# Performance work log

Hardware: AMD Instinct MI355X
Metric: run time of the kernel (lower is better)

The kernel has to match this reference:

```python
import jax, jax.numpy as jnp
import numpy as np

B, IH, IW = 16, 32, 32
N = IH * IW
HEADS, DIM_HEAD = 8, 64
INNER = HEADS * DIM_HEAD  # 512
INP, OUP = 512, 512
SCALE = DIM_HEAD ** -0.5


def _relative_index():
    # replicate torch.meshgrid (ij) -> coords [2, N]
    yy, xx = np.meshgrid(np.arange(IH), np.arange(IW), indexing='ij')
    coords = np.stack([yy.reshape(-1), xx.reshape(-1)])  # [2, N]
    rel = coords[:, :, None] - coords[:, None, :]        # [2, N, N]
    rel[0] += IH - 1
    rel[1] += IW - 1
    rel[0] *= 2 * IW - 1
    return jnp.asarray(rel.sum(0).reshape(-1), dtype=jnp.int32)  # [N*N]


def setup_inputs() -> dict:
    key = jax.random.key(0)
    k1, k2, k3, k4, k5 = jax.random.split(key, 5)
    x = jax.random.normal(k1, (B, N, INP), dtype=jnp.float32)
    W_qkv = jax.random.normal(k2, (INP, 3 * INNER), dtype=jnp.float32) * (INP ** -0.5)
    # table is initialized to zeros in the module; use small randn so bias path is exercised
    rel_table = jax.random.normal(k3, ((2 * IH - 1) * (2 * IW - 1), HEADS), dtype=jnp.float32) * 0.02
    W_out = jax.random.normal(k4, (INNER, OUP), dtype=jnp.float32) * (INNER ** -0.5)
    b_out = jax.random.normal(k5, (OUP,), dtype=jnp.float32) * 0.02
    return {
        'x': x,
        'W_qkv': W_qkv,
        'rel_table': rel_table,
        'W_out': W_out,
        'b_out': b_out,
        'rel_index': _relative_index(),
    }


def reference(x, W_qkv, rel_table, W_out, b_out, rel_index):
    b, n, _ = x.shape
    qkv = x @ W_qkv                                            # [b, n, 3*inner]
    q, k, v = jnp.split(qkv, 3, axis=-1)
    def to_heads(t):
        return t.reshape(b, n, HEADS, DIM_HEAD).transpose(0, 2, 1, 3)  # [b, h, n, d]
    q, k, v = to_heads(q), to_heads(k), to_heads(v)
    dots = jnp.einsum('bhnd,bhmd->bhnm', q, k) * SCALE         # [b, h, n, n]
    bias = rel_table[rel_index].reshape(n, n, HEADS).transpose(2, 0, 1)[None]  # [1, h, n, n]
    attn = jax.nn.softmax(dots + bias, axis=-1)
    out = jnp.einsum('bhnm,bhmd->bhnd', attn, v)               # [b, h, n, d]
    out = out.transpose(0, 2, 1, 3).reshape(b, n, INNER)       # [b, n, inner]
    return out @ W_out + b_out
```

## Files before the change

### kernel.cpp

```cpp
#include <hip/hip_runtime.h>
#include <math.h>

#define BATCH 16
#define NTOK 1024
#define HEADS 8
#define DHEAD 64
#define INNER 512
#define QKV_COLS 1536
#define SCALE_L2E 0.1803368801111244f
#define LOG2E 1.4426950408889634f

#if __has_builtin(__builtin_amdgcn_exp2f)
#define EXP2F(x) __builtin_amdgcn_exp2f(x)
#else
#define EXP2F(x) __expf((x) * 0.6931471805599453f)
#endif

typedef _Float16 f16x8 __attribute__((ext_vector_type(8)));
typedef _Float16 f16x4 __attribute__((ext_vector_type(4)));
typedef float f32x4 __attribute__((ext_vector_type(4)));

__device__ __forceinline__ void glds16(const void* g, void* l) {
    __builtin_amdgcn_global_load_lds(
        (const __attribute__((address_space(1))) unsigned int*)g,
        (__attribute__((address_space(3))) unsigned int*)l, 16, 0, 0);
}

#define XV (BATCH * NTOK * INNER / 4)
#define WQ (INNER * QKV_COLS)
#define WO (INNER * INNER)

__global__ __launch_bounds__(256)
void convert_inputs(const float* __restrict__ x, const float* __restrict__ Wq,
                    const float* __restrict__ Wo, _Float16* __restrict__ x_h,
                    _Float16* __restrict__ Wq_t, _Float16* __restrict__ Wo_t) {
    int idx = blockIdx.x * 256 + threadIdx.x;
    if (idx < XV) {
        float4 v = ((const float4*)x)[idx];
        f16x4 h;
        h[0] = (_Float16)v.x; h[1] = (_Float16)v.y;
        h[2] = (_Float16)v.z; h[3] = (_Float16)v.w;
        *(f16x4*)(x_h + (size_t)idx * 4) = h;
    } else if (idx < XV + WQ) {
        int i = idx - XV;
        int n = i >> 9, k = i & 511;
        Wq_t[i] = (_Float16)Wq[k * QKV_COLS + n];
    } else if (idx < XV + WQ + WO) {
        int i = idx - XV - WQ;
        int n = i >> 9, k = i & 511;
        Wo_t[i] = (_Float16)Wo[k * INNER + n];
    }
}

template<bool OUT_F16, bool ADD_BIAS>
__global__ __launch_bounds__(256)
void gemm_f16(const _Float16* __restrict__ A, const _Float16* __restrict__ Bt,
              const float* __restrict__ bias, void* __restrict__ Cout,
              int M, int N, int K) {
    __shared__ _Float16 As[128 * 32];
    __shared__ _Float16 Bs[128 * 32];

    const int t    = threadIdx.x;
    const int l    = t & 63;
    const int w    = t >> 6;
    const int wm   = w >> 1;
    const int wn   = w & 1;
    const int quad = l >> 4;
    const int lrow = l & 15;
    const size_t row0 = (size_t)blockIdx.y * 128;
    const size_t col0 = (size_t)blockIdx.x * 128;

    const int srow = t >> 2;
    const int sch  = t & 3;

    f32x4 acc[4][4] = {};

    for (int k0 = 0; k0 < K; k0 += 32) {
        __syncthreads();
        glds16(A + (row0 + srow) * K + k0 + sch * 8,            (char*)As + t * 16);
        glds16(A + (row0 + 64 + srow) * K + k0 + sch * 8,       (char*)As + 4096 + t * 16);
        glds16(Bt + (col0 + srow) * K + k0 + sch * 8,           (char*)Bs + t * 16);
        glds16(Bt + (col0 + 64 + srow) * K + k0 + sch * 8,      (char*)Bs + 4096 + t * 16);
        __syncthreads();

        f16x8 af[4], bf[4];
#pragma unroll
        for (int i = 0; i < 4; ++i)
            af[i] = *(const f16x8*)(As + (wm * 64 + i * 16 + lrow) * 32 + quad * 8);
#pragma unroll
        for (int j = 0; j < 4; ++j)
            bf[j] = *(const f16x8*)(Bs + (wn * 64 + j * 16 + lrow) * 32 + quad * 8);
#pragma unroll
        for (int i = 0; i < 4; ++i)
#pragma unroll
            for (int j = 0; j < 4; ++j)
                acc[i][j] = __builtin_amdgcn_mfma_f32_16x16x32_f16(af[i], bf[j], acc[i][j], 0, 0, 0);
    }

#pragma unroll
    for (int i = 0; i < 4; ++i) {
#pragma unroll
        for (int j = 0; j < 4; ++j) {
            size_t r = row0 + wm * 64 + i * 16 + quad * 4;
            size_t c = col0 + wn * 64 + j * 16 + lrow;
#pragma unroll
            for (int reg = 0; reg < 4; ++reg) {
                float v = acc[i][j][reg];
                if (OUT_F16) {
                    ((_Float16*)Cout)[(r + reg) * N + c] = (_Float16)v;
                } else {
                    if (ADD_BIAS) v += bias[c];
                    ((float*)Cout)[(r + reg) * N + c] = v;
                }
            }
        }
    }
}

__global__ __launch_bounds__(256)
void transpose_v(const _Float16* __restrict__ qkv, _Float16* __restrict__ vt) {
    __shared__ _Float16 T[64][72];
    const int t  = threadIdx.x;
    const int j0 = blockIdx.x * 64;
    const int h  = blockIdx.y, bb = blockIdx.z;
    const int jr = t >> 2;
    const int dc = (t & 3) * 16;
    const _Float16* src = qkv + ((size_t)bb * NTOK + j0 + jr) * QKV_COLS + 2 * INNER + h * DHEAD + dc;
    f16x8 v0 = *(const f16x8*)src;
    f16x8 v1 = *(const f16x8*)(src + 8);
#pragma unroll
    for (int e = 0; e < 8; ++e) { T[jr][dc + e] = v0[e]; T[jr][dc + 8 + e] = v1[e]; }
    __syncthreads();
    const int dr = t >> 2;
    const int jc = (t & 3) * 16;
    f16x8 o0, o1;
#pragma unroll
    for (int e = 0; e < 8; ++e) { o0[e] = T[jc + e][dr]; o1[e] = T[jc + 8 + e][dr]; }
    _Float16* dst = vt + (((size_t)bb * HEADS + h) * 64 + dr) * NTOK + j0 + jc;
    *(f16x8*)dst = o0;
    *(f16x8*)(dst + 8) = o1;
}

__global__ __launch_bounds__(256)
void attn_f16_v4(const _Float16* __restrict__ qkv, const _Float16* __restrict__ vt,
                 const float* __restrict__ rel_table, _Float16* __restrict__ out) {
    __shared__ _Float16 Ks[2][64 * 64];
    __shared__ _Float16 Vs[2][64 * 64];
    __shared__ _Float16 Ps[4][32 * 64];
    __shared__ float biasS[3969];

    const int t    = threadIdx.x;
    const int l    = t & 63;
    const int w    = t >> 6;
    const int quad = l >> 4;
    const int lrow = l & 15;
    const int h    = blockIdx.y;
    const int bb   = blockIdx.z;
    const int i0   = blockIdx.x * 128;
    const int qr0  = i0 + w * 32;

    for (int idx = t; idx < 3969; idx += 256)
        biasS[idx] = rel_table[idx * HEADS + h] * LOG2E;

    const size_t tokbase = (size_t)bb * NTOK;

    f16x8 aq[2][2];
#pragma unroll
    for (int mt = 0; mt < 2; ++mt)
#pragma unroll
        for (int ksi = 0; ksi < 2; ++ksi)
            aq[mt][ksi] = *(const f16x8*)(qkv + (tokbase + qr0 + mt * 16 + lrow) * QKV_COLS
                                          + h * DHEAD + ksi * 32 + quad * 8);

    f32x4 O[2][4];
    float lpart[2][4];
#pragma unroll
    for (int mt = 0; mt < 2; ++mt)
#pragma unroll
        for (int k = 0; k < 4; ++k) {
            O[mt][k] = (f32x4){0.f, 0.f, 0.f, 0.f};
            lpart[mt][k] = 0.f;
        }

    const int iyc = qr0 >> 5;
    const int ixb0 = quad * 4;
    const int ixb1 = 16 + quad * 4;

    const int kr  = t >> 3;
    const int ksl = t & 7;
    const _Float16* kbase = qkv + tokbase * QKV_COLS + INNER + h * DHEAD;
    const _Float16* vbase = vt + ((size_t)(bb * HEADS + h) * 64) * NTOK;

    auto stage = [&](int jt, int buf) {
        const int j0 = jt * 64;
        const int swz = (ksl ^ (kr & 7)) * 8;
        glds16(kbase + (size_t)(j0 + kr) * QKV_COLS + swz,      (char*)Ks[buf] + t * 16);
        glds16(kbase + (size_t)(j0 + 32 + kr) * QKV_COLS + swz, (char*)Ks[buf] + 4096 + t * 16);
        glds16(vbase + (size_t)kr * NTOK + j0 + swz,            (char*)Vs[buf] + t * 16);
        glds16(vbase + (size_t)(32 + kr) * NTOK + j0 + swz,     (char*)Vs[buf] + 4096 + t * 16);
    };

    stage(0, 0);

    _Float16* Pw = Ps[w];

    for (int jt = 0; jt < 16; ++jt) {
        const int buf = jt & 1;
        __syncthreads();
        if (jt < 15) stage(jt + 1, buf ^ 1);

        const int j0 = jt * 64;

        f32x4 S[2][4];
#pragma unroll
        for (int jn = 0; jn < 4; ++jn) {
            S[0][jn] = (f32x4){0.f, 0.f, 0.f, 0.f};
            S[1][jn] = (f32x4){0.f, 0.f, 0.f, 0.f};
            const int row = jn * 16 + lrow;
#pragma unroll
            for (int ksi = 0; ksi < 2; ++ksi) {
                f16x8 bk = *(const f16x8*)(Ks[buf] + row * 64 + (((ksi * 4 + quad) ^ (row & 7)) * 8));
#pragma unroll
                for (int mt = 0; mt < 2; ++mt)
                    S[mt][jn] = __builtin_amdgcn_mfma_f32_16x16x32_f16(aq[mt][ksi], bk, S[mt][jn], 0, 0, 0);
            }
        }

#pragma unroll
        for (int jn = 0; jn < 4; ++jn) {
            const int j  = j0 + jn * 16 + lrow;
            const int jy = j >> 5, jx = j & 31;
            const int rowoff = (iyc - jy + 31) * 63 - jx + 31;
#pragma unroll
            for (int mt = 0; mt < 2; ++mt) {
                const int idxbase = rowoff + (mt ? ixb1 : ixb0);
                float b0 = biasS[idxbase + 0];
                float b1 = biasS[idxbase + 1];
                float b2 = biasS[idxbase + 2];
                float b3 = biasS[idxbase + 3];
                const int mbase = mt * 16 + quad * 4;
                float p0 = EXP2F(fmaf(S[mt][jn][0], SCALE_L2E, b0));
                float p1 = EXP2F(fmaf(S[mt][jn][1], SCALE_L2E, b1));
                float p2 = EXP2F(fmaf(S[mt][jn][2], SCALE_L2E, b2));
                float p3 = EXP2F(fmaf(S[mt][jn][3], SCALE_L2E, b3));
                lpart[mt][0] += p0; lpart[mt][1] += p1;
                lpart[mt][2] += p2; lpart[mt][3] += p3;
                const int col = jn * 16 + lrow;
                const int csw = ((col >> 3) ^ ((mbase + 0) & 7)) * 8 + (col & 7);
                Pw[(mbase + 0) * 64 + (((col >> 3) ^ ((mbase + 0) & 7)) * 8) + (col & 7)] = (_Float16)p0;
                Pw[(mbase + 1) * 64 + (((col >> 3) ^ ((mbase + 1) & 7)) * 8) + (col & 7)] = (_Float16)p1;
                Pw[(mbase + 2) * 64 + (((col >> 3) ^ ((mbase + 2) & 7)) * 8) + (col & 7)] = (_Float16)p2;
                Pw[(mbase + 3) * 64 + (((col >> 3) ^ ((mbase + 3) & 7)) * 8) + (col & 7)] = (_Float16)p3;
                (void)csw;
            }
        }
        asm volatile("" ::: "memory");

#pragma unroll
        for (int ksi = 0; ksi < 2; ++ksi) {
            f16x8 ap[2];
#pragma unroll
            for (int mt = 0; mt < 2; ++mt) {
                const int arow = mt * 16 + lrow;
                ap[mt] = *(const f16x8*)(Pw + arow * 64 + (((ksi * 4 + quad) ^ (arow & 7)) * 8));
            }
#pragma unroll
            for (int dn = 0; dn < 4; ++dn) {
                const int d = dn * 16 + lrow;
                f16x8 bvv = *(const f16x8*)(Vs[buf] + d * 64 + (((ksi * 4 + quad) ^ (d & 7)) * 8));
#pragma unroll
                for (int mt = 0; mt < 2; ++mt)
                    O[mt][dn] = __builtin_amdgcn_mfma_f32_16x16x32_f16(ap[mt], bvv, O[mt][dn], 0, 0, 0);
            }
        }
    }

#pragma unroll
    for (int mt = 0; mt < 2; ++mt) {
#pragma unroll
        for (int r = 0; r < 4; ++r) {
            float s = lpart[mt][r];
#pragma unroll
            for (int off = 1; off < 16; off <<= 1)
                s += __shfl_xor(s, off);
            float inv = 1.f / s;
            const int i = qr0 + mt * 16 + quad * 4 + r;
#pragma unroll
            for (int dn = 0; dn < 4; ++dn)
                out[(tokbase + i) * INNER + h * DHEAD + dn * 16 + lrow] =
                    (_Float16)(O[mt][dn][r] * inv);
        }
    }
}

extern "C" void kernel_launch(void* const* d_in, const int* in_sizes, int n_in,
                              void* d_out, int out_size, void* d_ws, size_t ws_size,
                              hipStream_t stream) {
    const float* x         = (const float*)d_in[0];
    const float* W_qkv     = (const float*)d_in[1];
    const float* rel_table = (const float*)d_in[2];
    const float* W_out     = (const float*)d_in[3];
    const float* b_out     = (const float*)d_in[4];

    _Float16* x_h   = (_Float16*)d_ws;
    _Float16* Wq_t  = x_h + (size_t)BATCH * NTOK * INNER;
    _Float16* Wo_t  = Wq_t + (size_t)INNER * QKV_COLS;
    _Float16* qkv_h = Wo_t + (size_t)INNER * INNER;
    _Float16* att_h = qkv_h + (size_t)BATCH * NTOK * QKV_COLS;
    _Float16* vt_g  = att_h + (size_t)BATCH * NTOK * INNER;

    const int M = BATCH * NTOK;

    convert_inputs<<<(XV + WQ + WO + 255) / 256, 256, 0, stream>>>(
        x, W_qkv, W_out, x_h, Wq_t, Wo_t);

    gemm_f16<true, false><<<dim3(QKV_COLS / 128, M / 128), 256, 0, stream>>>(
        x_h, Wq_t, nullptr, qkv_h, M, QKV_COLS, INNER);

    transpose_v<<<dim3(NTOK / 64, HEADS, BATCH), 256, 0, stream>>>(qkv_h, vt_g);

    attn_f16_v4<<<dim3(NTOK / 128, HEADS, BATCH), 256, 0, stream>>>(
        qkv_h, vt_g, rel_table, att_h);

    gemm_f16<false, true><<<dim3(INNER / 128, M / 128), 256, 0, stream>>>(
        att_h, Wo_t, b_out, d_out, M, INNER, INNER);
}
```

Measured before the change: 243.8 us.

## Keep attention probabilities in registers via transposed MFMA, drop P shared-memory round trip

The attention kernel now computes S transposed (K as the A operand), so each lane's exp'd scores form the B operand of a 16x16x16 MFMA for P·V directly from registers. This removes the per-warp P staging buffer in shared memory and its store/load traffic. It also stores the bias table as fp16 and adds an occupancy hint of 4 blocks per CU. The trade-offs are twice as many smaller MFMAs for P·V, reduced bias precision, and possible register pressure under the tighter launch bound.

```diff
diff --git a/kernel.cpp b/kernel.cpp
--- a/kernel.cpp
+++ b/kernel.cpp
@@ -19,6 +19,9 @@
 typedef _Float16 f16x8 __attribute__((ext_vector_type(8)));
 typedef _Float16 f16x4 __attribute__((ext_vector_type(4)));
 typedef float f32x4 __attribute__((ext_vector_type(4)));
+
+#define MFMA32(a, b, c) __builtin_amdgcn_mfma_f32_16x16x32_f16(a, b, c, 0, 0, 0)
+#define MFMA16(a, b, c) __builtin_amdgcn_mfma_f32_16x16x16f16(a, b, c, 0, 0, 0)
 
 __device__ __forceinline__ void glds16(const void* g, void* l) {
     __builtin_amdgcn_global_load_lds(
@@ -141,13 +144,12 @@
     *(f16x8*)(dst + 8) = o1;
 }
 
-__global__ __launch_bounds__(256)
-void attn_f16_v4(const _Float16* __restrict__ qkv, const _Float16* __restrict__ vt,
+__global__ __launch_bounds__(256, 4)
+void attn_f16_v5(const _Float16* __restrict__ qkv, const _Float16* __restrict__ vt,
                  const float* __restrict__ rel_table, _Float16* __restrict__ out) {
     __shared__ _Float16 Ks[2][64 * 64];
     __shared__ _Float16 Vs[2][64 * 64];
-    __shared__ _Float16 Ps[4][32 * 64];
-    __shared__ float biasS[3969];
+    __shared__ _Float16 biasH[3969];
 
     const int t    = threadIdx.x;
     const int l    = t & 63;
@@ -156,11 +158,10 @@
     const int lrow = l & 15;
     const int h    = blockIdx.y;
     const int bb   = blockIdx.z;
-    const int i0   = blockIdx.x * 128;
-    const int qr0  = i0 + w * 32;
+    const int qr0  = blockIdx.x * 128 + w * 32;
 
     for (int idx = t; idx < 3969; idx += 256)
-        biasS[idx] = rel_table[idx * HEADS + h] * LOG2E;
+        biasH[idx] = (_Float16)(rel_table[idx * HEADS + h] * LOG2E);
 
     const size_t tokbase = (size_t)bb * NTOK;
 
@@ -172,123 +173,90 @@
             aq[mt][ksi] = *(const f16x8*)(qkv + (tokbase + qr0 + mt * 16 + lrow) * QKV_COLS
                                           + h * DHEAD + ksi * 32 + quad * 8);
 
-    f32x4 O[2][4];
-    float lpart[2][4];
-#pragma unroll
-    for (int mt = 0; mt < 2; ++mt)
-#pragma unroll
-        for (int k = 0; k < 4; ++k) {
-            O[mt][k] = (f32x4){0.f, 0.f, 0.f, 0.f};
-            lpart[mt][k] = 0.f;
-        }
-
-    const int iyc = qr0 >> 5;
-    const int ixb0 = quad * 4;
-    const int ixb1 = 16 + quad * 4;
+    f32x4 O[2][4] = {};
+    float l0 = 0.f, l1 = 0.f;
+
+    const int bconst = ((qr0 >> 5) + 31) * 63 + 31 + lrow - quad * 4;
 
     const int kr  = t >> 3;
     const int ksl = t & 7;
     const _Float16* kbase = qkv + tokbase * QKV_COLS + INNER + h * DHEAD;
     const _Float16* vbase = vt + ((size_t)(bb * HEADS + h) * 64) * NTOK;
 
-    auto stage = [&](int jt, int buf) {
-        const int j0 = jt * 64;
+    auto stage = [&](int jt, int bufi) {
+        const int j0s = jt * 64;
         const int swz = (ksl ^ (kr & 7)) * 8;
-        glds16(kbase + (size_t)(j0 + kr) * QKV_COLS + swz,      (char*)Ks[buf] + t * 16);
-        glds16(kbase + (size_t)(j0 + 32 + kr) * QKV_COLS + swz, (char*)Ks[buf] + 4096 + t * 16);
-        glds16(vbase + (size_t)kr * NTOK + j0 + swz,            (char*)Vs[buf] + t * 16);
-        glds16(vbase + (size_t)(32 + kr) * NTOK + j0 + swz,     (char*)Vs[buf] + 4096 + t * 16);
+        glds16(kbase + (size_t)(j0s + kr) * QKV_COLS + swz,      (char*)Ks[bufi] + t * 16);
+        glds16(kbase + (size_t)(j0s + 32 + kr) * QKV_COLS + swz, (char*)Ks[bufi] + 4096 + t * 16);
+        glds16(vbase + (size_t)kr * NTOK + j0s + swz,            (char*)Vs[bufi] + t * 16);
+        glds16(vbase + (size_t)(32 + kr) * NTOK + j0s + swz,     (char*)Vs[bufi] + 4096 + t * 16);
     };
 
     stage(0, 0);
-
-    _Float16* Pw = Ps[w];
 
     for (int jt = 0; jt < 16; ++jt) {
         const int buf = jt & 1;
         __syncthreads();
         if (jt < 15) stage(jt + 1, buf ^ 1);
 
-        const int j0 = jt * 64;
-
-        f32x4 S[2][4];
 #pragma unroll
         for (int jn = 0; jn < 4; ++jn) {
-            S[0][jn] = (f32x4){0.f, 0.f, 0.f, 0.f};
-            S[1][jn] = (f32x4){0.f, 0.f, 0.f, 0.f};
             const int row = jn * 16 + lrow;
+            f32x4 S0 = {}, S1 = {};
 #pragma unroll
             for (int ksi = 0; ksi < 2; ++ksi) {
                 f16x8 bk = *(const f16x8*)(Ks[buf] + row * 64 + (((ksi * 4 + quad) ^ (row & 7)) * 8));
-#pragma unroll
-                for (int mt = 0; mt < 2; ++mt)
-                    S[mt][jn] = __builtin_amdgcn_mfma_f32_16x16x32_f16(aq[mt][ksi], bk, S[mt][jn], 0, 0, 0);
-            }
-        }
-
-#pragma unroll
-        for (int jn = 0; jn < 4; ++jn) {
-            const int j  = j0 + jn * 16 + lrow;
-            const int jy = j >> 5, jx = j & 31;
-            const int rowoff = (iyc - jy + 31) * 63 - jx + 31;
-#pragma unroll
-            for (int mt = 0; mt < 2; ++mt) {
-                const int idxbase = rowoff + (mt ? ixb1 : ixb0);
-                float b0 = biasS[idxbase + 0];
-                float b1 = biasS[idxbase + 1];
-                float b2 = biasS[idxbase + 2];
-                float b3 = biasS[idxbase + 3];
-                const int mbase = mt * 16 + quad * 4;
-                float p0 = EXP2F(fmaf(S[mt][jn][0], SCALE_L2E, b0));
-                float p1 = EXP2F(fmaf(S[mt][jn][1], SCALE_L2E, b1));
-                float p2 = EXP2F(fmaf(S[mt][jn][2], SCALE_L2E, b2));
-                float p3 = EXP2F(fmaf(S[mt][jn][3], SCALE_L2E, b3));
-                lpart[mt][0] += p0; lpart[mt][1] += p1;
-                lpart[mt][2] += p2; lpart[mt][3] += p3;
-                const int col = jn * 16 + lrow;
-                const int csw = ((col >> 3) ^ ((mbase + 0) & 7)) * 8 + (col & 7);
-                Pw[(mbase + 0) * 64 + (((col >> 3) ^ ((mbase + 0) & 7)) * 8) + (col & 7)] = (_Float16)p0;
-                Pw[(mbase + 1) * 64 + (((col >> 3) ^ ((mbase + 1) & 7)) * 8) + (col & 7)] = (_Float16)p1;
-                Pw[(mbase + 2) * 64 + (((col >> 3) ^ ((mbase + 2) & 7)) * 8) + (col & 7)] = (_Float16)p2;
-                Pw[(mbase + 3) * 64 + (((col >> 3) ^ ((mbase + 3) & 7)) * 8) + (col & 7)] = (_Float16)p3;
-                (void)csw;
-            }
-        }
-        asm volatile("" ::: "memory");
-
-#pragma unroll
-        for (int ksi = 0; ksi < 2; ++ksi) {
-            f16x8 ap[2];
-#pragma unroll
-            for (int mt = 0; mt < 2; ++mt) {
-                const int arow = mt * 16 + lrow;
-                ap[mt] = *(const f16x8*)(Pw + arow * 64 + (((ksi * 4 + quad) ^ (arow & 7)) * 8));
-            }
+                S0 = MFMA32(bk, aq[0][ksi], S0);
+                S1 = MFMA32(bk, aq[1][ksi], S1);
+            }
+
+            const int base0 = bconst - (jt * 2 + (jn >> 1)) * 63 - (jn & 1) * 16;
+            f16x4 pb0, pb1;
+            {
+                float p0 = EXP2F(fmaf(S0[0], SCALE_L2E, (float)biasH[base0 - 0]));
+                float p1 = EXP2F(fmaf(S0[1], SCALE_L2E, (float)biasH[base0 - 1]));
+                float p2 = EXP2F(fmaf(S0[2], SCALE_L2E, (float)biasH[base0 - 2]));
+                float p3 = EXP2F(fmaf(S0[3], SCALE_L2E, (float)biasH[base0 - 3]));
+                l0 += (p0 + p1) + (p2 + p3);
+                pb0[0] = (_Float16)p0; pb0[1] = (_Float16)p1;
+                pb0[2] = (_Float16)p2; pb0[3] = (_Float16)p3;
+            }
+            {
+                const int base1 = base0 + 16;
+                float p0 = EXP2F(fmaf(S1[0], SCALE_L2E, (float)biasH[base1 - 0]));
+                float p1 = EXP2F(fmaf(S1[1], SCALE_L2E, (float)biasH[base1 - 1]));
+                float p2 = EXP2F(fmaf(S1[2], SCALE_L2E, (float)biasH[base1 - 2]));
+                float p3 = EXP2F(fmaf(S1[3], SCALE_L2E, (float)biasH[base1 - 3]));
+                l1 += (p0 + p1) + (p2 + p3);
+                pb1[0] = (_Float16)p0; pb1[1] = (_Float16)p1;
+                pb1[2] = (_Float16)p2; pb1[3] = (_Float16)p3;
+            }
+
 #pragma unroll
             for (int dn = 0; dn < 4; ++dn) {
                 const int d = dn * 16 + lrow;
-                f16x8 bvv = *(const f16x8*)(Vs[buf] + d * 64 + (((ksi * 4 + quad) ^ (d & 7)) * 8));
-#pragma unroll
-                for (int mt = 0; mt < 2; ++mt)
-                    O[mt][dn] = __builtin_amdgcn_mfma_f32_16x16x32_f16(ap[mt], bvv, O[mt][dn], 0, 0, 0);
+                f16x4 av = *(const f16x4*)(Vs[buf] + d * 64
+                              + (((jn * 2 + (quad >> 1)) ^ (d & 7)) * 8) + (quad & 1) * 4);
+                O[0][dn] = MFMA16(av, pb0, O[0][dn]);
+                O[1][dn] = MFMA16(av, pb1, O[1][dn]);
             }
         }
     }
 
 #pragma unroll
     for (int mt = 0; mt < 2; ++mt) {
-#pragma unroll
-        for (int r = 0; r < 4; ++r) {
-            float s = lpart[mt][r];
-#pragma unroll
-            for (int off = 1; off < 16; off <<= 1)
-                s += __shfl_xor(s, off);
-            float inv = 1.f / s;
-            const int i = qr0 + mt * 16 + quad * 4 + r;
-#pragma unroll
-            for (int dn = 0; dn < 4; ++dn)
-                out[(tokbase + i) * INNER + h * DHEAD + dn * 16 + lrow] =
-                    (_Float16)(O[mt][dn][r] * inv);
+        float s = mt ? l1 : l0;
+        s += __shfl_xor(s, 16);
+        s += __shfl_xor(s, 32);
+        const float inv = 1.f / s;
+        const size_t orow = (tokbase + qr0 + mt * 16 + lrow) * INNER + h * DHEAD;
+#pragma unroll
+        for (int dn = 0; dn < 4; ++dn) {
+            const f32x4 o = O[mt][dn];
+            f16x4 ov;
+            ov[0] = (_Float16)(o[0] * inv); ov[1] = (_Float16)(o[1] * inv);
+            ov[2] = (_Float16)(o[2] * inv); ov[3] = (_Float16)(o[3] * inv);
+            *(f16x4*)(out + orow + dn * 16 + quad * 4) = ov;
         }
     }
 }
@@ -319,7 +287,7 @@
 
     transpose_v<<<dim3(NTOK / 64, HEADS, BATCH), 256, 0, stream>>>(qkv_h, vt_g);
 
-    attn_f16_v4<<<dim3(NTOK / 128, HEADS, BATCH), 256, 0, stream>>>(
+    attn_f16_v5<<<dim3(NTOK / 128, HEADS, BATCH), 256, 0, stream>>>(
         qkv_h, vt_g, rel_table, att_h);
 
     gemm_f16<false, true><<<dim3(INNER / 128, M / 128), 256, 0, stream>>>(
```

Result: no change. 243.5 us (-0.1%).
